# Optimization experiments

Hardware: AMD Instinct MI355X
Metric: run time of the kernel (lower is better)

The kernel has to match this reference:

```python
import jax, jax.numpy as jnp
import numpy as np

NUM_HEADS = 8
Q_DIM = 32  # == k_dim == v_dim (required by the broadcasted matmul in the source)

def _conv1x1(x, w, b):
    # x: [B, C, H, W]; w: [O, C]; b: [O]  (1x1 conv == channel matmul)
    return jnp.einsum('bchw,oc->bohw', x, w) + b[None, :, None, None]

def setup_inputs() -> dict:
    key = jax.random.key(0)
    ks = jax.random.split(key, 7)
    B, C, H, W = 16, 256, 64, 64
    O = Q_DIM * NUM_HEADS  # 256
    s = 1.0 / np.sqrt(C)
    return {
        'x':  jax.random.normal(ks[0], (B, C, H, W), jnp.float32),
        'wq': jax.random.normal(ks[1], (O, C), jnp.float32) * s,
        'bq': jax.random.normal(ks[2], (O,), jnp.float32) * 0.01,
        'wk': jax.random.normal(ks[3], (O, C), jnp.float32) * s,
        'bk': jax.random.normal(ks[4], (O,), jnp.float32) * 0.01,
        'wv': jax.random.normal(ks[5], (O, C), jnp.float32) * s,
        'bv': jax.random.normal(ks[6], (O,), jnp.float32) * 0.01,
    }

def reference(x, wq, bq, wk, bk, wv, bv):
    B, C, H, W = x.shape
    nH, d = NUM_HEADS, Q_DIM
    q = _conv1x1(x, wq, bq).reshape(B, nH, d, H, W)
    k = _conv1x1(x, wk, bk).reshape(B, nH, d, H, W)
    v = _conv1x1(x, wv, bv).reshape(B, nH, d, H, W)
    # torch.matmul(q, k.transpose(-2,-1)): contract over width, batched over (B, nH, d)
    scores = jnp.einsum('bndhw,bndgw->bndhg', q, k) / jnp.sqrt(jnp.asarray(d, x.dtype))
    weights = jax.nn.softmax(scores, axis=-1)  # [B, nH, d, H, H]
    ctx = jnp.einsum('bndhg,bndgw->bndhw', weights, v)
    return ctx.reshape(B, nH * d, H, W)
```

## Files before the change

kernel.cpp:

```cpp
#include <hip/hip_runtime.h>
#include <stdint.h>

#define LOG2E       1.4426950408889634f
#define INV_SQRT32  0.17677669529663687f

using bf16x8 = __attribute__((ext_vector_type(8))) short;
using f32x4  = __attribute__((ext_vector_type(4))) float;

__device__ __forceinline__ unsigned short f2bf(float f) {
  union { float f; uint32_t u; } v; v.f = f;
  uint32_t r = v.u + 0x7fffu + ((v.u >> 16) & 1u);
  return (unsigned short)(r >> 16);
}

typedef const __attribute__((address_space(1))) void* gas_ptr;
typedef __attribute__((address_space(3))) void*       las_ptr;
__device__ __forceinline__ void load_lds16(const void* g, void* l) {
  __builtin_amdgcn_global_load_lds((gas_ptr)g, (las_ptr)l, 16, 0, 0);
}

__global__ __launch_bounds__(256) void convert_w(
    const float* __restrict__ wq, const float* __restrict__ bq,
    const float* __restrict__ wk, const float* __restrict__ bk,
    const float* __restrict__ wv, const float* __restrict__ bv,
    unsigned short* __restrict__ Wcat, float* __restrict__ biasc) {
  int idx = (blockIdx.x * 256 + threadIdx.x) * 4;
  int p = idx >> 16;
  int rem = idx & 0xffff;
  const float* src = (p == 0) ? wq : (p == 1) ? wk : wv;
  float4 v = *(const float4*)(src + rem);
  ushort4 o;
  o.x = f2bf(v.x); o.y = f2bf(v.y); o.z = f2bf(v.z); o.w = f2bf(v.w);
  *(ushort4*)(Wcat + idx) = o;
  if (blockIdx.x < 3) {
    const float* sb = (blockIdx.x == 0) ? bq : (blockIdx.x == 1) ? bk : bv;
    biasc[blockIdx.x * 256 + threadIdx.x] = sb[threadIdx.x];
  }
}

__global__ __launch_bounds__(256) void transpose_x(const float* __restrict__ x,
                                                   unsigned short* __restrict__ xt) {
  __shared__ float tile[64 * 65];
  int b = blockIdx.z;
  int s0 = blockIdx.x * 64, c0 = blockIdx.y * 64;
  int t = threadIdx.x;
  int sl = t & 63, g = t >> 6;
  const float* xp = x + ((size_t)(b * 256 + c0)) * 4096 + s0 + sl;
#pragma unroll
  for (int ii = 0; ii < 16; ++ii) {
    int cl = g * 16 + ii;
    tile[cl * 65 + sl] = xp[(size_t)cl * 4096];
  }
  __syncthreads();
#pragma unroll
  for (int jj = 0; jj < 16; ++jj) {
    int s_loc = g * 16 + jj;
    float v = tile[sl * 65 + s_loc];
    xt[((size_t)(b * 4096 + s0 + s_loc)) * 256 + c0 + sl] = f2bf(v);
  }
}

__global__ __launch_bounds__(256) void gemm_qkv(
    const unsigned short* __restrict__ Wc, const float* __restrict__ biasc,
    const unsigned short* __restrict__ Xt, unsigned short* __restrict__ qkv) {
  __shared__ unsigned short As[128 * 32];
  __shared__ unsigned short Bs[128 * 32];
  int blk = blockIdx.x;
  int b = blk / 192;
  int rest = blk - b * 192;
  int mt = rest >> 5, nt = rest & 31;
  int m0 = mt * 128, n0 = nt * 128;
  int tid = threadIdx.x;
  int lane = tid & 63, wave = tid >> 6;
  int quad = lane >> 4, rt = lane & 15;
  int wm = wave >> 1, wn = wave & 1;

  f32x4 acc[4][4];
#pragma unroll
  for (int i = 0; i < 4; ++i)
#pragma unroll
    for (int j = 0; j < 4; ++j) acc[i][j] = (f32x4){0.f, 0.f, 0.f, 0.f};

  int lr = lane >> 2;
  int lk = (lane & 3) * 8;
  const unsigned short* gA0 = Wc + (size_t)(m0 + (wave * 2 + 0) * 16 + lr) * 256 + lk;
  const unsigned short* gA1 = Wc + (size_t)(m0 + (wave * 2 + 1) * 16 + lr) * 256 + lk;
  const unsigned short* gB0 = Xt + ((size_t)b * 4096 + n0 + (wave * 2 + 0) * 16 + lr) * 256 + lk;
  const unsigned short* gB1 = Xt + ((size_t)b * 4096 + n0 + (wave * 2 + 1) * 16 + lr) * 256 + lk;
  unsigned short* lA0 = &As[(wave * 2 + 0) * 16 * 32];
  unsigned short* lA1 = &As[(wave * 2 + 1) * 16 * 32];
  unsigned short* lB0 = &Bs[(wave * 2 + 0) * 16 * 32];
  unsigned short* lB1 = &Bs[(wave * 2 + 1) * 16 * 32];

#pragma unroll
  for (int kc = 0; kc < 8; ++kc) {
    int ko = kc * 32;
    load_lds16(gA0 + ko, lA0);
    load_lds16(gA1 + ko, lA1);
    load_lds16(gB0 + ko, lB0);
    load_lds16(gB1 + ko, lB1);
    __syncthreads();
    bf16x8 af[4], bfr[4];
#pragma unroll
    for (int mi = 0; mi < 4; ++mi)
      af[mi] = *(const bf16x8*)&As[(wm * 64 + mi * 16 + rt) * 32 + quad * 8];
#pragma unroll
    for (int ni = 0; ni < 4; ++ni)
      bfr[ni] = *(const bf16x8*)&Bs[(wn * 64 + ni * 16 + rt) * 32 + quad * 8];
#pragma unroll
    for (int mi = 0; mi < 4; ++mi)
#pragma unroll
      for (int ni = 0; ni < 4; ++ni)
        acc[mi][ni] = __builtin_amdgcn_mfma_f32_16x16x32_bf16(af[mi], bfr[ni], acc[mi][ni], 0, 0, 0);
    __syncthreads();
  }

  size_t obase = (size_t)b * 768;
#pragma unroll
  for (int mi = 0; mi < 4; ++mi) {
    int o = m0 + wm * 64 + mi * 16 + quad * 4;
    float bsv[4];
#pragma unroll
    for (int r = 0; r < 4; ++r) bsv[r] = biasc[o + r];
#pragma unroll
    for (int ni = 0; ni < 4; ++ni) {
      int s = n0 + wn * 64 + ni * 16 + rt;
#pragma unroll
      for (int r = 0; r < 4; ++r)
        qkv[(obase + o + r) * 4096 + s] = f2bf(acc[mi][ni][r] + bsv[r]);
    }
  }
}

__global__ __launch_bounds__(256) void attn(const unsigned short* __restrict__ qkv,
                                            float* __restrict__ out) {
  __shared__ char sh[36608];
  unsigned short* Qs = (unsigned short*)sh;
  unsigned short* Ks = (unsigned short*)(sh + 9216);
  float*          Sf = (float*)sh;
  unsigned short* Ps = (unsigned short*)(sh + 16640);
  unsigned short* Vt = (unsigned short*)(sh + 25856);
  float* red    = (float*)(sh + 35072);
  float* rowmax = (float*)(sh + 36096);
  float* rowinv = (float*)(sh + 36352);

  int blk = blockIdx.x;
  int b = blk >> 8, o = blk & 255;
  int t = threadIdx.x;
  size_t base = ((size_t)b * 768 + o) * 4096;
  const unsigned short* qg = qkv + base;
  const unsigned short* kg = qkv + base + (size_t)256 * 4096;
  const unsigned short* vg = qkv + base + (size_t)512 * 4096;

  {
    int h = t >> 2, w0 = (t & 3) * 16;
    const uint4* qp = (const uint4*)(qg + h * 64 + w0);
    const uint4* kp = (const uint4*)(kg + h * 64 + w0);
    uint4 q0 = qp[0], q1 = qp[1];
    uint4 k0 = kp[0], k1 = kp[1];
    *(uint4*)&Qs[h * 72 + w0]     = q0;
    *(uint4*)&Qs[h * 72 + w0 + 8] = q1;
    *(uint4*)&Ks[h * 72 + w0]     = k0;
    *(uint4*)&Ks[h * 72 + w0 + 8] = k1;

    int w = t & 63, gb = (t >> 6) * 16;
    unsigned short vv[16];
#pragma unroll
    for (int j = 0; j < 16; ++j) vv[j] = vg[(size_t)(gb + j) * 64 + w];
    *(uint4*)&Vt[w * 72 + gb]     = ((uint4*)vv)[0];
    *(uint4*)&Vt[w * 72 + gb + 8] = ((uint4*)vv)[1];
  }
  __syncthreads();

  int lane = t & 63, wave = t >> 6;
  int rt = lane & 15, quad = lane >> 4;
  int wm = wave >> 1, wn = wave & 1;

  f32x4 accs[2][2];
#pragma unroll
  for (int i = 0; i < 2; ++i)
#pragma unroll
    for (int j = 0; j < 2; ++j) accs[i][j] = (f32x4){0.f, 0.f, 0.f, 0.f};
#pragma unroll
  for (int ks = 0; ks < 2; ++ks) {
    int kk = ks * 32 + quad * 8;
    bf16x8 a0 = *(const bf16x8*)&Qs[(wm * 32 + rt) * 72 + kk];
    bf16x8 a1 = *(const bf16x8*)&Qs[(wm * 32 + 16 + rt) * 72 + kk];
    bf16x8 b0 = *(const bf16x8*)&Ks[(wn * 32 + rt) * 72 + kk];
    bf16x8 b1 = *(const bf16x8*)&Ks[(wn * 32 + 16 + rt) * 72 + kk];
    accs[0][0] = __builtin_amdgcn_mfma_f32_16x16x32_bf16(a0, b0, accs[0][0], 0, 0, 0);
    accs[0][1] = __builtin_amdgcn_mfma_f32_16x16x32_bf16(a0, b1, accs[0][1], 0, 0, 0);
    accs[1][0] = __builtin_amdgcn_mfma_f32_16x16x32_bf16(a1, b0, accs[1][0], 0, 0, 0);
    accs[1][1] = __builtin_amdgcn_mfma_f32_16x16x32_bf16(a1, b1, accs[1][1], 0, 0, 0);
  }
  __syncthreads();

#pragma unroll
  for (int tm = 0; tm < 2; ++tm)
#pragma unroll
    for (int tn = 0; tn < 2; ++tn)
#pragma unroll
      for (int r = 0; r < 4; ++r)
        Sf[(wm * 32 + tm * 16 + quad * 4 + r) * 65 + wn * 32 + tn * 16 + rt] =
            accs[tm][tn][r] * INV_SQRT32;
  __syncthreads();

  int hr = t & 63, qt = t >> 6;
  float s[16];
#pragma unroll
  for (int e = 0; e < 16; ++e) s[e] = Sf[hr * 65 + qt * 16 + e];
  float m = s[0];
#pragma unroll
  for (int e = 1; e < 16; ++e) m = fmaxf(m, s[e]);
  red[qt * 64 + hr] = m;
  __syncthreads();
  if (t < 64)
    rowmax[t] = fmaxf(fmaxf(red[t], red[64 + t]), fmaxf(red[128 + t], red[192 + t]));
  __syncthreads();
  float mr = rowmax[hr];
  float ssum = 0.f;
  unsigned short pv[16];
#pragma unroll
  for (int e = 0; e < 16; ++e) {
    float p = exp2f((s[e] - mr) * LOG2E);
    ssum += p;
    pv[e] = f2bf(p);
  }
  *(uint4*)&Ps[hr * 72 + qt * 16]     = ((uint4*)pv)[0];
  *(uint4*)&Ps[hr * 72 + qt * 16 + 8] = ((uint4*)pv)[1];
  red[qt * 64 + hr] = ssum;
  __syncthreads();
  if (t < 64) rowinv[t] = 1.f / (red[t] + red[64 + t] + red[128 + t] + red[192 + t]);
  __syncthreads();

  f32x4 acco[2][2];
#pragma unroll
  for (int i = 0; i < 2; ++i)
#pragma unroll
    for (int j = 0; j < 2; ++j) acco[i][j] = (f32x4){0.f, 0.f, 0.f, 0.f};
#pragma unroll
  for (int ks = 0; ks < 2; ++ks) {
    int kk = ks * 32 + quad * 8;
    bf16x8 a0 = *(const bf16x8*)&Ps[(wm * 32 + rt) * 72 + kk];
    bf16x8 a1 = *(const bf16x8*)&Ps[(wm * 32 + 16 + rt) * 72 + kk];
    bf16x8 b0 = *(const bf16x8*)&Vt[(wn * 32 + rt) * 72 + kk];
    bf16x8 b1 = *(const bf16x8*)&Vt[(wn * 32 + 16 + rt) * 72 + kk];
    acco[0][0] = __builtin_amdgcn_mfma_f32_16x16x32_bf16(a0, b0, acco[0][0], 0, 0, 0);
    acco[0][1] = __builtin_amdgcn_mfma_f32_16x16x32_bf16(a0, b1, acco[0][1], 0, 0, 0);
    acco[1][0] = __builtin_amdgcn_mfma_f32_16x16x32_bf16(a1, b0, acco[1][0], 0, 0, 0);
    acco[1][1] = __builtin_amdgcn_mfma_f32_16x16x32_bf16(a1, b1, acco[1][1], 0, 0, 0);
  }

  float* op = out + ((size_t)(b * 256 + o)) * 4096;
#pragma unroll
  for (int tm = 0; tm < 2; ++tm) {
#pragma unroll
    for (int r = 0; r < 4; ++r) {
      int h = wm * 32 + tm * 16 + quad * 4 + r;
      float inv = rowinv[h];
#pragma unroll
      for (int tn = 0; tn < 2; ++tn) {
        int w = wn * 32 + tn * 16 + rt;
        op[h * 64 + w] = acco[tm][tn][r] * inv;
      }
    }
  }
}

extern "C" void kernel_launch(void* const* d_in, const int* in_sizes, int n_in,
                              void* d_out, int out_size, void* d_ws, size_t ws_size,
                              hipStream_t stream) {
  const float* x  = (const float*)d_in[0];
  const float* wq = (const float*)d_in[1];
  const float* bq = (const float*)d_in[2];
  const float* wk = (const float*)d_in[3];
  const float* bk = (const float*)d_in[4];
  const float* wv = (const float*)d_in[5];
  const float* bv = (const float*)d_in[6];
  float* out = (float*)d_out;

  char* ws = (char*)d_ws;
  unsigned short* Wcat  = (unsigned short*)ws;
  float*          biasc = (float*)(ws + 393216);
  unsigned short* Xt    = (unsigned short*)(ws + 396288);
  unsigned short* qkv   = (unsigned short*)(ws + 396288 + 33554432);

  hipLaunchKernelGGL(convert_w, dim3(192), dim3(256), 0, stream,
                     wq, bq, wk, bk, wv, bv, Wcat, biasc);
  hipLaunchKernelGGL(transpose_x, dim3(64, 4, 16), dim3(256), 0, stream, x, Xt);
  hipLaunchKernelGGL(gemm_qkv, dim3(3072), dim3(256), 0, stream, Wcat, biasc, Xt, qkv);
  hipLaunchKernelGGL(attn, dim3(4096), dim3(256), 0, stream, qkv, out);
}
```

Baseline: 201.1 us.

## Double-buffer QKV GEMM LDS, swizzle LDS layout, remap blocks, vectorize transpose stores

The QKV projection GEMM now double-buffers its LDS tiles, issuing the next k-chunk's global-to-LDS loads before the MFMAs on the current chunk, so load latency can overlap compute. LDS rows are XOR-swizzled on both the write and read side to cut bank conflicts. Block indices are remapped to interleave batches across XCDs for cache locality. The x transpose kernel now writes 16-byte packed bf16 stores instead of scalar 2-byte stores. LDS use doubles, and with a single barrier per iteration the double buffer depends on the barrier ordering to stay correct.

```diff
diff --git a/kernel.cpp b/kernel.cpp
--- a/kernel.cpp
+++ b/kernel.cpp
@@ -53,19 +53,23 @@
   }
   __syncthreads();
 #pragma unroll
-  for (int jj = 0; jj < 16; ++jj) {
-    int s_loc = g * 16 + jj;
-    float v = tile[sl * 65 + s_loc];
-    xt[((size_t)(b * 4096 + s0 + s_loc)) * 256 + c0 + sl] = f2bf(v);
+  for (int it = 0; it < 2; ++it) {
+    int idx = it * 256 + t;
+    int s_loc = idx >> 3, cb = (idx & 7) * 8;
+    unsigned short ov[8];
+#pragma unroll
+    for (int j = 0; j < 8; ++j) ov[j] = f2bf(tile[(cb + j) * 65 + s_loc]);
+    *(uint4*)&xt[((size_t)(b * 4096 + s0 + s_loc)) * 256 + c0 + cb] = *(uint4*)ov;
   }
 }
 
 __global__ __launch_bounds__(256) void gemm_qkv(
     const unsigned short* __restrict__ Wc, const float* __restrict__ biasc,
     const unsigned short* __restrict__ Xt, unsigned short* __restrict__ qkv) {
-  __shared__ unsigned short As[128 * 32];
-  __shared__ unsigned short Bs[128 * 32];
+  __shared__ unsigned short As[2][128 * 32];
+  __shared__ unsigned short Bs[2][128 * 32];
   int blk = blockIdx.x;
+  blk = (blk & 7) * 384 + (blk >> 3);
   int b = blk / 192;
   int rest = blk - b * 192;
   int mt = rest >> 5, nt = rest & 31;
@@ -82,38 +86,44 @@
     for (int j = 0; j < 4; ++j) acc[i][j] = (f32x4){0.f, 0.f, 0.f, 0.f};
 
   int lr = lane >> 2;
-  int lk = (lane & 3) * 8;
-  const unsigned short* gA0 = Wc + (size_t)(m0 + (wave * 2 + 0) * 16 + lr) * 256 + lk;
-  const unsigned short* gA1 = Wc + (size_t)(m0 + (wave * 2 + 1) * 16 + lr) * 256 + lk;
-  const unsigned short* gB0 = Xt + ((size_t)b * 4096 + n0 + (wave * 2 + 0) * 16 + lr) * 256 + lk;
-  const unsigned short* gB1 = Xt + ((size_t)b * 4096 + n0 + (wave * 2 + 1) * 16 + lr) * 256 + lk;
-  unsigned short* lA0 = &As[(wave * 2 + 0) * 16 * 32];
-  unsigned short* lA1 = &As[(wave * 2 + 1) * 16 * 32];
-  unsigned short* lB0 = &Bs[(wave * 2 + 0) * 16 * 32];
-  unsigned short* lB1 = &Bs[(wave * 2 + 1) * 16 * 32];
-
+  int sl_src = (lane & 3) ^ ((lane >> 3) & 3);
+  const unsigned short* gA0 = Wc + (size_t)(m0 + wave * 32 + lr) * 256 + sl_src * 8;
+  const unsigned short* gA1 = gA0 + 16 * 256;
+  const unsigned short* gB0 = Xt + ((size_t)b * 4096 + n0 + wave * 32 + lr) * 256 + sl_src * 8;
+  const unsigned short* gB1 = gB0 + 16 * 256;
+
+#define STAGE(bufi, ko)                                        \
+  do {                                                         \
+    load_lds16(gA0 + (ko), &As[bufi][wave * 1024]);            \
+    load_lds16(gA1 + (ko), &As[bufi][wave * 1024 + 512]);      \
+    load_lds16(gB0 + (ko), &Bs[bufi][wave * 1024]);            \
+    load_lds16(gB1 + (ko), &Bs[bufi][wave * 1024 + 512]);      \
+  } while (0)
+
+  STAGE(0, 0);
+  __syncthreads();
+
+  int cur = 0;
+  int rsw = (quad ^ ((rt >> 1) & 3)) * 8;
 #pragma unroll
   for (int kc = 0; kc < 8; ++kc) {
-    int ko = kc * 32;
-    load_lds16(gA0 + ko, lA0);
-    load_lds16(gA1 + ko, lA1);
-    load_lds16(gB0 + ko, lB0);
-    load_lds16(gB1 + ko, lB1);
-    __syncthreads();
+    if (kc < 7) STAGE(cur ^ 1, (kc + 1) * 32);
     bf16x8 af[4], bfr[4];
 #pragma unroll
     for (int mi = 0; mi < 4; ++mi)
-      af[mi] = *(const bf16x8*)&As[(wm * 64 + mi * 16 + rt) * 32 + quad * 8];
+      af[mi] = *(const bf16x8*)&As[cur][(wm * 64 + mi * 16 + rt) * 32 + rsw];
 #pragma unroll
     for (int ni = 0; ni < 4; ++ni)
-      bfr[ni] = *(const bf16x8*)&Bs[(wn * 64 + ni * 16 + rt) * 32 + quad * 8];
+      bfr[ni] = *(const bf16x8*)&Bs[cur][(wn * 64 + ni * 16 + rt) * 32 + rsw];
 #pragma unroll
     for (int mi = 0; mi < 4; ++mi)
 #pragma unroll
       for (int ni = 0; ni < 4; ++ni)
         acc[mi][ni] = __builtin_amdgcn_mfma_f32_16x16x32_bf16(af[mi], bfr[ni], acc[mi][ni], 0, 0, 0);
     __syncthreads();
-  }
+    cur ^= 1;
+  }
+#undef STAGE
 
   size_t obase = (size_t)b * 768;
 #pragma unroll
```

Result: no change. 199.7 us (-0.7%).
